# Optimization experiments

Measured on AMD Instinct MI355X. Metric: run time of the kernel, lower is better.

The kernel has to match this reference:

```python
import jax, jax.numpy as jnp
import numpy as np

B, S, D, H = 2, 2048, 1024, 16
HD = D // H  # head_dim = 64


def setup_inputs() -> dict:
    key = jax.random.key(0)
    ks = jax.random.split(key, 6)
    scale = D ** -0.5
    x = jax.random.normal(ks[0], (B, S, D), dtype=jnp.float32)
    wq = jax.random.normal(ks[1], (D, D), dtype=jnp.float32) * scale
    wk = jax.random.normal(ks[2], (D, D), dtype=jnp.float32) * scale
    wv = jax.random.normal(ks[3], (D, D), dtype=jnp.float32) * scale
    wo = jax.random.normal(ks[4], (D, D), dtype=jnp.float32) * scale
    # RoPE frequencies: theta_i = 10000^(-2i/HD), angles[t, i] = t * theta_i
    inv_freq = 1.0 / (10000.0 ** (np.arange(0, HD, 2, dtype=np.float32) / HD))
    t = np.arange(S, dtype=np.float32)
    angles = np.outer(t, inv_freq)  # [S, HD//2]
    freqs_cos = jnp.asarray(np.cos(angles), dtype=jnp.float32)
    freqs_sin = jnp.asarray(np.sin(angles), dtype=jnp.float32)
    # additive causal mask [1,1,S,S]
    neg = jnp.float32(-1e9)
    mask = jnp.triu(jnp.full((S, S), neg, dtype=jnp.float32), k=1)[None, None]
    return {"x": x, "wq": wq, "wk": wk, "wv": wv, "wo": wo,
            "freqs_cos": freqs_cos, "freqs_sin": freqs_sin,
            "mask": mask, "start_pos": 0}


def _apply_rope(q, freqs_cos, freqs_sin):
    # q: [B, S, H, HD] -> pairs (even, odd) rotated by angle per position
    b, s, h, hd = q.shape
    q2 = q.reshape(b, s, h, hd // 2, 2)
    qr, qi = q2[..., 0], q2[..., 1]
    c = freqs_cos[None, :, None, :]  # [1, S, 1, HD//2]
    sn = freqs_sin[None, :, None, :]
    out_r = qr * c - qi * sn
    out_i = qr * sn + qi * c
    return jnp.stack([out_r, out_i], axis=-1).reshape(b, s, h, hd)


def reference(x, wq, wk, wv, wo, freqs_cos, freqs_sin, mask, start_pos):
    b, s, _ = x.shape
    xq = (x @ wq).reshape(b, s, H, HD)
    xk = (x @ wk).reshape(b, s, H, HD)
    xv = (x @ wv).reshape(b, s, H, HD)
    xq = _apply_rope(xq, freqs_cos, freqs_sin)
    xk = _apply_rope(xk, freqs_cos, freqs_sin)
    # [B, H, S, HD]
    q = xq.transpose(0, 2, 1, 3)
    k = xk.transpose(0, 2, 1, 3)
    v = xv.transpose(0, 2, 1, 3)
    scores = jnp.einsum('bhqd,bhkd->bhqk', q, k) / jnp.sqrt(jnp.float32(HD))
    scores = scores + mask
    probs = jax.nn.softmax(scores.astype(jnp.float32), axis=-1).astype(q.dtype)
    out = jnp.einsum('bhqk,bhkd->bhqd', probs, v)
    out = out.transpose(0, 2, 1, 3).reshape(b, s, H * HD)
    return out @ wo
```

## Files before the change

### kernel.cpp

```cpp
#include <hip/hip_runtime.h>

typedef unsigned short u16;
typedef __bf16 bf16x8 __attribute__((ext_vector_type(8)));
typedef float f32x4 __attribute__((ext_vector_type(4)));

#define DD 1024
#define SS 2048
#define HH 16
#define HDIM 64

__device__ __forceinline__ u16 f2bf(float f) {
  union { float f; unsigned u; } x; x.f = f;
  unsigned r = x.u + 0x7FFFu + ((x.u >> 16) & 1u);
  return (u16)(r >> 16);
}

__device__ __forceinline__ u16 f2bf_s(float f) {
  unsigned r;
  asm("v_cvt_pk_bf16_f32 %0, %1, %2" : "=v"(r) : "v"(f), "v"(0.f));
  return (u16)r;
}

__device__ __forceinline__ void gload_lds16(const u16* g, u16* l) {
  __builtin_amdgcn_global_load_lds((const __attribute__((address_space(1))) void*)g,
                                   (__attribute__((address_space(3))) void*)l, 16, 0, 0);
}

__global__ __launch_bounds__(256) void cvt_x(const float* __restrict__ in, u16* __restrict__ out, int n) {
  int i = (blockIdx.x * 256 + threadIdx.x) * 4;
  if (i + 3 < n) {
    float4 v = *(const float4*)(in + i);
    out[i + 0] = f2bf(v.x);
    out[i + 1] = f2bf(v.y);
    out[i + 2] = f2bf(v.z);
    out[i + 3] = f2bf(v.w);
  }
}

__global__ __launch_bounds__(256) void transpose_w(const float* __restrict__ w0, const float* __restrict__ w1,
                                                   const float* __restrict__ w2, const float* __restrict__ w3,
                                                   u16* __restrict__ out) {
  __shared__ float t[32][33];
  const float* w = (blockIdx.z == 0) ? w0 : (blockIdx.z == 1) ? w1 : (blockIdx.z == 2) ? w2 : w3;
  u16* o = out + (size_t)blockIdx.z * DD * DD;
  int j0 = blockIdx.x * 32;
  int i0 = blockIdx.y * 32;
  int tx = threadIdx.x, ty = threadIdx.y;
#pragma unroll
  for (int r = ty; r < 32; r += 8)
    t[r][tx] = w[(size_t)(i0 + r) * DD + j0 + tx];
  __syncthreads();
#pragma unroll
  for (int r = ty; r < 32; r += 8)
    o[(size_t)(j0 + r) * DD + i0 + tx] = f2bf(t[tx][r]);
}

__global__ __launch_bounds__(512, 4) void gemm_qkv(const u16* __restrict__ xb, const u16* __restrict__ wT,
                                                   const float* __restrict__ fc, const float* __restrict__ fs,
                                                   u16* __restrict__ Qr, u16* __restrict__ Kr, u16* __restrict__ Vt) {
  __shared__ u16 As[2][128 * 64];
  __shared__ u16 Bs[2][192 * 64];
  const int tid = threadIdx.x;
  const int lane = tid & 63, wid = tid >> 6;
  const int wm = wid >> 2, wn = wid & 3;
  const int lr = lane & 15, lg = lane >> 4;
  const int m0 = blockIdx.x * 128, n0 = blockIdx.y * 192;

  f32x4 acc[4][3];
#pragma unroll
  for (int i = 0; i < 4; ++i)
#pragma unroll
    for (int j = 0; j < 3; ++j) acc[i][j] = (f32x4){0.f, 0.f, 0.f, 0.f};

  auto stage = [&](int buf, int k0) {
#pragma unroll
    for (int i = 0; i < 2; ++i) {
      int c = tid + i * 512;
      int row = c >> 3, j = (c & 7) ^ (row & 7);
      gload_lds16(xb + (size_t)(m0 + row) * DD + k0 + j * 8, &As[buf][c * 8]);
    }
#pragma unroll
    for (int i = 0; i < 3; ++i) {
      int c = tid + i * 512;
      int row = c >> 3, j = (c & 7) ^ (row & 7);
      gload_lds16(wT + (size_t)(n0 + row) * DD + k0 + j * 8, &Bs[buf][c * 8]);
    }
  };

  stage(0, 0);
  for (int kt = 0; kt < 16; ++kt) {
    const int cur = kt & 1;
    __syncthreads();
    if (kt < 15) stage(cur ^ 1, (kt + 1) * 64);
#pragma unroll
    for (int ks = 0; ks < 2; ++ks) {
      bf16x8 af[4], bfr[3];
#pragma unroll
      for (int mi = 0; mi < 4; ++mi) {
        int row = wm * 64 + mi * 16 + lr;
        int ch = (ks * 4 + lg) ^ (row & 7);
        af[mi] = *(const bf16x8*)(&As[cur][row * 64 + ch * 8]);
      }
#pragma unroll
      for (int ni = 0; ni < 3; ++ni) {
        int row = wn * 48 + ni * 16 + lr;
        int ch = (ks * 4 + lg) ^ (row & 7);
        bfr[ni] = *(const bf16x8*)(&Bs[cur][row * 64 + ch * 8]);
      }
      __builtin_amdgcn_s_setprio(1);
#pragma unroll
      for (int mi = 0; mi < 4; ++mi)
#pragma unroll
        for (int ni = 0; ni < 3; ++ni)
          acc[mi][ni] = __builtin_amdgcn_mfma_f32_16x16x32_bf16(af[mi], bfr[ni], acc[mi][ni], 0, 0, 0);
      __builtin_amdgcn_s_setprio(0);
    }
  }

#pragma unroll
  for (int mi = 0; mi < 4; ++mi)
#pragma unroll
    for (int ni = 0; ni < 3; ++ni) {
      const int nb = n0 + wn * 48 + ni * 16;
      const int z = nb >> 10;
      const int nn = (nb & 1023) + lr;
      const int h = nn >> 6, hd = nn & 63;
#pragma unroll
      for (int j = 0; j < 4; ++j) {
        int m = m0 + wm * 64 + mi * 16 + lg * 4 + j;
        float v = acc[mi][ni][j];
        int b = m >> 11, s = m & 2047;
        if (z == 2) {
          Vt[((size_t)(b * HH + h) * HDIM + hd) * SS + s] = f2bf(v);
        } else {
          float pv = __shfl_xor(v, 1);
          int fi = s * 32 + (hd >> 1);
          float c = fc[fi], sn = fs[fi];
          float o = ((hd & 1) == 0) ? (v * c - pv * sn) : (pv * sn + v * c);
          u16* dst = (z == 0) ? Qr : Kr;
          dst[((size_t)(b * HH + h) * SS + s) * HDIM + hd] = f2bf(o);
        }
      }
    }
}

__device__ __forceinline__ void stage_tile(const u16* __restrict__ Kh, const u16* __restrict__ Vh,
                                           int i2, u16* Kbuf, u16* Vbuf, int tid) {
#pragma unroll
  for (int k = 0; k < 2; ++k) {
    const int c = tid + k * 512;
    const int tt = c >> 9, cl = c & 511;
    const int row = cl >> 3, j = (cl & 7) ^ (row & 7);
    gload_lds16(Kh + (size_t)(i2 * 128 + tt * 64 + row) * HDIM + j * 8, Kbuf + c * 8);
    gload_lds16(Vh + (size_t)row * SS + i2 * 128 + tt * 64 + j * 8, Vbuf + c * 8);
  }
}

__device__ __forceinline__ void attn_pass(int qt, int bh, const u16* __restrict__ Qh,
                                          const u16* __restrict__ Kh, const u16* __restrict__ Vh,
                                          u16* __restrict__ Ob, u16* KbR, u16* VbR, u16* Pw,
                                          int gid, int wq) {
  const int tid = threadIdx.x;
  const int lane = tid & 63;
  const int lr = lane & 15, lg = lane >> 4;
  const int q0 = qt * 64 + wq * 16;

  bf16x8 aq[2];
#pragma unroll
  for (int ks = 0; ks < 2; ++ks)
    aq[ks] = *(const bf16x8*)(Qh + (q0 + lr) * HDIM + ks * 32 + lg * 8);

  bf16x8 ones;
  {
    union { u16 u[8]; bf16x8 v; } ou;
#pragma unroll
    for (int i = 0; i < 8; ++i) ou.u[i] = 0x3F80;
    ones = ou.v;
  }

  f32x4 o[4];
#pragma unroll
  for (int d = 0; d < 4; ++d) o[d] = (f32x4){0.f, 0.f, 0.f, 0.f};
  f32x4 ls = (f32x4){0.f, 0.f, 0.f, 0.f};

  const int n2 = (qt + 2) >> 1;

  __syncthreads();
  stage_tile(Kh, Vh, 0, KbR, VbR, tid);

  for (int i = 0; i < n2; ++i) {
    const int cur = i & 1;
    __syncthreads();
    if (i + 1 < n2) stage_tile(Kh, Vh, i + 1, KbR + (cur ^ 1) * 8192, VbR + (cur ^ 1) * 8192, tid);

    const int t = 2 * i + gid;
    const u16* Kt = KbR + cur * 8192 + gid * 4096;
    const u16* Vtl = VbR + cur * 8192 + gid * 4096;

    f32x4 sc[4];
#pragma unroll
    for (int kb = 0; kb < 4; ++kb) sc[kb] = (f32x4){0.f, 0.f, 0.f, 0.f};
    __builtin_amdgcn_s_setprio(1);
#pragma unroll
    for (int ks = 0; ks < 2; ++ks)
#pragma unroll
      for (int kb = 0; kb < 4; ++kb) {
        int row = kb * 16 + lr;
        int ch = (ks * 4 + lg) ^ (row & 7);
        bf16x8 bk = *(const bf16x8*)(Kt + row * 64 + ch * 8);
        sc[kb] = __builtin_amdgcn_mfma_f32_16x16x32_bf16(aq[ks], bk, sc[kb], 0, 0, 0);
      }
    __builtin_amdgcn_s_setprio(0);

    if (t >= qt) {
#pragma unroll
      for (int kb = 0; kb < 4; ++kb)
#pragma unroll
        for (int j = 0; j < 4; ++j) {
          int q = q0 + lg * 4 + j;
          int kk = t * 64 + kb * 16 + lr;
          float e = __expf(sc[kb][j] * 0.125f);
          sc[kb][j] = (kk > q) ? 0.f : e;
        }
    } else {
#pragma unroll
      for (int kb = 0; kb < 4; ++kb)
#pragma unroll
        for (int j = 0; j < 4; ++j)
          sc[kb][j] = __expf(sc[kb][j] * 0.125f);
    }

#pragma unroll
    for (int kb = 0; kb < 4; ++kb)
#pragma unroll
      for (int j = 0; j < 4; ++j) {
        int rr = lg * 4 + j;
        int ccol = kb * 16 + lr;
        int ch = (ccol >> 3) ^ (rr & 7);
        Pw[rr * 64 + ch * 8 + (ccol & 7)] = f2bf_s(sc[kb][j]);
      }
#pragma unroll
    for (int ks = 0; ks < 2; ++ks) {
      int chp = (ks * 4 + lg) ^ (lr & 7);
      bf16x8 ap = *(const bf16x8*)(Pw + lr * 64 + chp * 8);
      __builtin_amdgcn_s_setprio(1);
      ls = __builtin_amdgcn_mfma_f32_16x16x32_bf16(ap, ones, ls, 0, 0, 0);
#pragma unroll
      for (int d = 0; d < 4; ++d) {
        int row = d * 16 + lr;
        int ch = (ks * 4 + lg) ^ (row & 7);
        bf16x8 bv = *(const bf16x8*)(Vtl + row * 64 + ch * 8);
        o[d] = __builtin_amdgcn_mfma_f32_16x16x32_bf16(ap, bv, o[d], 0, 0, 0);
      }
      __builtin_amdgcn_s_setprio(0);
    }
  }

  __syncthreads();
  float* mo = (float*)KbR;
  float* ml = (float*)VbR;
  if (gid == 1) {
#pragma unroll
    for (int d = 0; d < 4; ++d)
#pragma unroll
      for (int j = 0; j < 4; ++j)
        mo[(wq * 16 + lg * 4 + j) * 64 + d * 16 + lr] = o[d][j];
    if (lr == 0) {
#pragma unroll
      for (int j = 0; j < 4; ++j) ml[wq * 16 + lg * 4 + j] = ls[j];
    }
  }
  __syncthreads();
  if (gid == 0) {
    const int b = bh >> 4, h = bh & 15;
#pragma unroll
    for (int j = 0; j < 4; ++j) ls[j] += ml[wq * 16 + lg * 4 + j];
#pragma unroll
    for (int d = 0; d < 4; ++d)
#pragma unroll
      for (int j = 0; j < 4; ++j) {
        float val = o[d][j] + mo[(wq * 16 + lg * 4 + j) * 64 + d * 16 + lr];
        int s = q0 + lg * 4 + j;
        int col = h * HDIM + d * 16 + lr;
        Ob[((size_t)b * SS + s) * DD + col] = f2bf(val / ls[j]);
      }
  }
}

__global__ __launch_bounds__(512, 4) void attn(const u16* __restrict__ Qr, const u16* __restrict__ Kr,
                                               const u16* __restrict__ Vt, u16* __restrict__ Ob) {
  __shared__ u16 Kb[2][2][64 * 64];
  __shared__ u16 Vb[2][2][64 * 64];
  __shared__ u16 Ps[8][16 * 64];
  const int id = blockIdx.x;
  const int xcd = id & 7;
  const int r = id >> 3;
  const int pair = r & 15;
  const int bh = xcd * 4 + (r >> 4);
  const u16* Qh = Qr + (size_t)bh * SS * HDIM;
  const u16* Kh = Kr + (size_t)bh * SS * HDIM;
  const u16* Vh = Vt + (size_t)bh * HDIM * SS;
  const int wid = threadIdx.x >> 6;
  const int gid = wid >> 2, wq = wid & 3;
  u16* Pw = &Ps[wid][0];
  attn_pass(pair, bh, Qh, Kh, Vh, Ob, &Kb[0][0][0], &Vb[0][0][0], Pw, gid, wq);
  attn_pass(31 - pair, bh, Qh, Kh, Vh, Ob, &Kb[0][0][0], &Vb[0][0][0], Pw, gid, wq);
}

__global__ __launch_bounds__(256, 2) void gemm_wo(const u16* __restrict__ Ab, const u16* __restrict__ woT,
                                                  float* __restrict__ out) {
  __shared__ u16 As[2][128 * 64];
  __shared__ u16 Bs[2][128 * 64];
  const int tid = threadIdx.x;
  const int lane = tid & 63, wid = tid >> 6;
  const int wm = wid >> 1, wn = wid & 1;
  const int lr = lane & 15, lg = lane >> 4;
  const int m0 = blockIdx.x * 128, n0 = blockIdx.y * 128;

  f32x4 acc[4][4];
#pragma unroll
  for (int i = 0; i < 4; ++i)
#pragma unroll
    for (int j = 0; j < 4; ++j) acc[i][j] = (f32x4){0.f, 0.f, 0.f, 0.f};

  auto stage = [&](int buf, int k0) {
#pragma unroll
    for (int i = 0; i < 4; ++i) {
      int c = i * 256 + tid;
      int row = c >> 3, j = (c & 7) ^ (row & 7);
      gload_lds16(Ab + (size_t)(m0 + row) * DD + k0 + j * 8, &As[buf][c * 8]);
      gload_lds16(woT + (size_t)(n0 + row) * DD + k0 + j * 8, &Bs[buf][c * 8]);
    }
  };

  stage(0, 0);
  for (int kt = 0; kt < 16; ++kt) {
    const int cur = kt & 1;
    __syncthreads();
    if (kt < 15) stage(cur ^ 1, (kt + 1) * 64);
#pragma unroll
    for (int ks = 0; ks < 2; ++ks) {
      bf16x8 af[4], bfr[4];
#pragma unroll
      for (int mi = 0; mi < 4; ++mi) {
        int row = wm * 64 + mi * 16 + lr;
        int ch = (ks * 4 + lg) ^ (row & 7);
        af[mi] = *(const bf16x8*)(&As[cur][row * 64 + ch * 8]);
      }
#pragma unroll
      for (int ni = 0; ni < 4; ++ni) {
        int row = wn * 64 + ni * 16 + lr;
        int ch = (ks * 4 + lg) ^ (row & 7);
        bfr[ni] = *(const bf16x8*)(&Bs[cur][row * 64 + ch * 8]);
      }
      __builtin_amdgcn_s_setprio(1);
#pragma unroll
      for (int mi = 0; mi < 4; ++mi)
#pragma unroll
        for (int ni = 0; ni < 4; ++ni)
          acc[mi][ni] = __builtin_amdgcn_mfma_f32_16x16x32_bf16(af[mi], bfr[ni], acc[mi][ni], 0, 0, 0);
      __builtin_amdgcn_s_setprio(0);
    }
  }

  const int lane2 = threadIdx.x & 63;
  (void)lane2;
#pragma unroll
  for (int mi = 0; mi < 4; ++mi)
#pragma unroll
    for (int ni = 0; ni < 4; ++ni)
#pragma unroll
      for (int j = 0; j < 4; ++j) {
        int m = m0 + wm * 64 + mi * 16 + lg * 4 + j;
        int n = n0 + wn * 64 + ni * 16 + lr;
        out[(size_t)m * DD + n] = acc[mi][ni][j];
      }
}

extern "C" void kernel_launch(void* const* d_in, const int* in_sizes, int n_in,
                              void* d_out, int out_size, void* d_ws, size_t ws_size,
                              hipStream_t stream) {
  const float* x  = (const float*)d_in[0];
  const float* wq = (const float*)d_in[1];
  const float* wk = (const float*)d_in[2];
  const float* wv = (const float*)d_in[3];
  const float* wo = (const float*)d_in[4];
  const float* fc = (const float*)d_in[5];
  const float* fs = (const float*)d_in[6];
  float* out = (float*)d_out;

  char* ws = (char*)d_ws;
  u16* xb = (u16*)(ws);
  u16* wT = (u16*)(ws + (8ull << 20));
  u16* Qr = (u16*)(ws + (16ull << 20));
  u16* Kr = (u16*)(ws + (24ull << 20));
  u16* Vt = (u16*)(ws + (32ull << 20));
  u16* Ob = (u16*)(ws + (40ull << 20));

  cvt_x<<<4096, 256, 0, stream>>>(x, xb, 4096 * 1024);
  transpose_w<<<dim3(32, 32, 4), dim3(32, 8), 0, stream>>>(wq, wk, wv, wo, wT);
  gemm_qkv<<<dim3(32, 16), 512, 0, stream>>>(xb, wT, fc, fs, Qr, Kr, Vt);
  attn<<<512, 512, 0, stream>>>(Qr, Kr, Vt, Ob);
  gemm_wo<<<dim3(32, 8), 256, 0, stream>>>(Ob, wT + 3ull * DD * DD, out);
}
```

Measured before the change: 118.6 us.

## Triple-buffer GEMM K-loops with vmcnt waits, fuse prep kernels, widen gemm_wo

Both GEMMs move from double to triple LDS buffering. Each iteration issues the next tile's global-to-LDS loads, waits only on the older tile with a partial s_waitcnt vmcnt, then does a single barrier, which removes one full sync and lets the load overlap the MFMA work. The x cast and weight-transpose kernels are merged into one launch to cut a kernel launch. gemm_wo goes from 256 to 512 threads with half the accumulators per wave. The trade-off is more LDS per block, which may lower occupancy (gemm_qkv's launch bound drops to 2 blocks per SM), and the hand-counted vmcnt values must match the number of loads issued.

```diff
diff --git a/kernel.cpp b/kernel.cpp
--- a/kernel.cpp
+++ b/kernel.cpp
@@ -26,26 +26,30 @@
                                    (__attribute__((address_space(3))) void*)l, 16, 0, 0);
 }
 
-__global__ __launch_bounds__(256) void cvt_x(const float* __restrict__ in, u16* __restrict__ out, int n) {
-  int i = (blockIdx.x * 256 + threadIdx.x) * 4;
-  if (i + 3 < n) {
-    float4 v = *(const float4*)(in + i);
-    out[i + 0] = f2bf(v.x);
-    out[i + 1] = f2bf(v.y);
-    out[i + 2] = f2bf(v.z);
-    out[i + 3] = f2bf(v.w);
-  }
-}
-
-__global__ __launch_bounds__(256) void transpose_w(const float* __restrict__ w0, const float* __restrict__ w1,
-                                                   const float* __restrict__ w2, const float* __restrict__ w3,
-                                                   u16* __restrict__ out) {
+__global__ __launch_bounds__(256) void prep(const float* __restrict__ x,
+                                            const float* __restrict__ w0, const float* __restrict__ w1,
+                                            const float* __restrict__ w2, const float* __restrict__ w3,
+                                            u16* __restrict__ xb, u16* __restrict__ wT) {
   __shared__ float t[32][33];
-  const float* w = (blockIdx.z == 0) ? w0 : (blockIdx.z == 1) ? w1 : (blockIdx.z == 2) ? w2 : w3;
-  u16* o = out + (size_t)blockIdx.z * DD * DD;
-  int j0 = blockIdx.x * 32;
-  int i0 = blockIdx.y * 32;
-  int tx = threadIdx.x, ty = threadIdx.y;
+  const int id = blockIdx.x;
+  const int tid = threadIdx.x;
+  if (id < 4096) {
+    int i = (id * 256 + tid) * 4;
+    float4 v = *(const float4*)(x + i);
+    xb[i + 0] = f2bf(v.x);
+    xb[i + 1] = f2bf(v.y);
+    xb[i + 2] = f2bf(v.z);
+    xb[i + 3] = f2bf(v.w);
+    return;
+  }
+  const int tt = id - 4096;
+  const int z = tt >> 10;
+  const int xy = tt & 1023;
+  const int j0 = (xy & 31) * 32;
+  const int i0 = (xy >> 5) * 32;
+  const float* w = (z == 0) ? w0 : (z == 1) ? w1 : (z == 2) ? w2 : w3;
+  u16* o = wT + (size_t)z * DD * DD;
+  const int tx = tid & 31, ty = tid >> 5;
 #pragma unroll
   for (int r = ty; r < 32; r += 8)
     t[r][tx] = w[(size_t)(i0 + r) * DD + j0 + tx];
@@ -55,11 +59,11 @@
     o[(size_t)(j0 + r) * DD + i0 + tx] = f2bf(t[tx][r]);
 }
 
-__global__ __launch_bounds__(512, 4) void gemm_qkv(const u16* __restrict__ xb, const u16* __restrict__ wT,
+__global__ __launch_bounds__(512, 2) void gemm_qkv(const u16* __restrict__ xb, const u16* __restrict__ wT,
                                                    const float* __restrict__ fc, const float* __restrict__ fs,
                                                    u16* __restrict__ Qr, u16* __restrict__ Kr, u16* __restrict__ Vt) {
-  __shared__ u16 As[2][128 * 64];
-  __shared__ u16 Bs[2][192 * 64];
+  __shared__ u16 As[3][128 * 64];
+  __shared__ u16 Bs[3][192 * 64];
   const int tid = threadIdx.x;
   const int lane = tid & 63, wid = tid >> 6;
   const int wm = wid >> 2, wn = wid & 3;
@@ -88,10 +92,17 @@
   };
 
   stage(0, 0);
+  int cur = 0;
   for (int kt = 0; kt < 16; ++kt) {
-    const int cur = kt & 1;
-    __syncthreads();
-    if (kt < 15) stage(cur ^ 1, (kt + 1) * 64);
+    if (kt < 15) {
+      int nxt = (cur == 2) ? 0 : cur + 1;
+      stage(nxt, (kt + 1) * 64);
+      asm volatile("s_waitcnt vmcnt(5)" ::: "memory");
+    } else {
+      asm volatile("s_waitcnt vmcnt(0)" ::: "memory");
+    }
+    __builtin_amdgcn_s_barrier();
+    __builtin_amdgcn_sched_barrier(0);
 #pragma unroll
     for (int ks = 0; ks < 2; ++ks) {
       bf16x8 af[4], bfr[3];
@@ -115,6 +126,7 @@
           acc[mi][ni] = __builtin_amdgcn_mfma_f32_16x16x32_bf16(af[mi], bfr[ni], acc[mi][ni], 0, 0, 0);
       __builtin_amdgcn_s_setprio(0);
     }
+    cur = (cur == 2) ? 0 : cur + 1;
   }
 
 #pragma unroll
@@ -307,26 +319,26 @@
   attn_pass(31 - pair, bh, Qh, Kh, Vh, Ob, &Kb[0][0][0], &Vb[0][0][0], Pw, gid, wq);
 }
 
-__global__ __launch_bounds__(256, 2) void gemm_wo(const u16* __restrict__ Ab, const u16* __restrict__ woT,
+__global__ __launch_bounds__(512, 2) void gemm_wo(const u16* __restrict__ Ab, const u16* __restrict__ woT,
                                                   float* __restrict__ out) {
-  __shared__ u16 As[2][128 * 64];
-  __shared__ u16 Bs[2][128 * 64];
+  __shared__ u16 As[3][128 * 64];
+  __shared__ u16 Bs[3][128 * 64];
   const int tid = threadIdx.x;
   const int lane = tid & 63, wid = tid >> 6;
   const int wm = wid >> 1, wn = wid & 1;
   const int lr = lane & 15, lg = lane >> 4;
   const int m0 = blockIdx.x * 128, n0 = blockIdx.y * 128;
 
-  f32x4 acc[4][4];
-#pragma unroll
-  for (int i = 0; i < 4; ++i)
+  f32x4 acc[2][4];
+#pragma unroll
+  for (int i = 0; i < 2; ++i)
 #pragma unroll
     for (int j = 0; j < 4; ++j) acc[i][j] = (f32x4){0.f, 0.f, 0.f, 0.f};
 
   auto stage = [&](int buf, int k0) {
 #pragma unroll
-    for (int i = 0; i < 4; ++i) {
-      int c = i * 256 + tid;
+    for (int i = 0; i < 2; ++i) {
+      int c = tid + i * 512;
       int row = c >> 3, j = (c & 7) ^ (row & 7);
       gload_lds16(Ab + (size_t)(m0 + row) * DD + k0 + j * 8, &As[buf][c * 8]);
       gload_lds16(woT + (size_t)(n0 + row) * DD + k0 + j * 8, &Bs[buf][c * 8]);
@@ -334,16 +346,23 @@
   };
 
   stage(0, 0);
+  int cur = 0;
   for (int kt = 0; kt < 16; ++kt) {
-    const int cur = kt & 1;
-    __syncthreads();
-    if (kt < 15) stage(cur ^ 1, (kt + 1) * 64);
+    if (kt < 15) {
+      int nxt = (cur == 2) ? 0 : cur + 1;
+      stage(nxt, (kt + 1) * 64);
+      asm volatile("s_waitcnt vmcnt(4)" ::: "memory");
+    } else {
+      asm volatile("s_waitcnt vmcnt(0)" ::: "memory");
+    }
+    __builtin_amdgcn_s_barrier();
+    __builtin_amdgcn_sched_barrier(0);
 #pragma unroll
     for (int ks = 0; ks < 2; ++ks) {
-      bf16x8 af[4], bfr[4];
-#pragma unroll
-      for (int mi = 0; mi < 4; ++mi) {
-        int row = wm * 64 + mi * 16 + lr;
+      bf16x8 af[2], bfr[4];
+#pragma unroll
+      for (int mi = 0; mi < 2; ++mi) {
+        int row = wm * 32 + mi * 16 + lr;
         int ch = (ks * 4 + lg) ^ (row & 7);
         af[mi] = *(const bf16x8*)(&As[cur][row * 64 + ch * 8]);
       }
@@ -355,23 +374,22 @@
       }
       __builtin_amdgcn_s_setprio(1);
 #pragma unroll
-      for (int mi = 0; mi < 4; ++mi)
+      for (int mi = 0; mi < 2; ++mi)
 #pragma unroll
         for (int ni = 0; ni < 4; ++ni)
           acc[mi][ni] = __builtin_amdgcn_mfma_f32_16x16x32_bf16(af[mi], bfr[ni], acc[mi][ni], 0, 0, 0);
       __builtin_amdgcn_s_setprio(0);
     }
-  }
-
-  const int lane2 = threadIdx.x & 63;
-  (void)lane2;
-#pragma unroll
-  for (int mi = 0; mi < 4; ++mi)
+    cur = (cur == 2) ? 0 : cur + 1;
+  }
+
+#pragma unroll
+  for (int mi = 0; mi < 2; ++mi)
 #pragma unroll
     for (int ni = 0; ni < 4; ++ni)
 #pragma unroll
       for (int j = 0; j < 4; ++j) {
-        int m = m0 + wm * 64 + mi * 16 + lg * 4 + j;
+        int m = m0 + wm * 32 + mi * 16 + lg * 4 + j;
         int n = n0 + wn * 64 + ni * 16 + lr;
         out[(size_t)m * DD + n] = acc[mi][ni][j];
       }
@@ -397,9 +415,8 @@
   u16* Vt = (u16*)(ws + (32ull << 20));
   u16* Ob = (u16*)(ws + (40ull << 20));
 
-  cvt_x<<<4096, 256, 0, stream>>>(x, xb, 4096 * 1024);
-  transpose_w<<<dim3(32, 32, 4), dim3(32, 8), 0, stream>>>(wq, wk, wv, wo, wT);
+  prep<<<8192, 256, 0, stream>>>(x, wq, wk, wv, wo, xb, wT);
   gemm_qkv<<<dim3(32, 16), 512, 0, stream>>>(xb, wT, fc, fs, Qr, Kr, Vt);
   attn<<<512, 512, 0, stream>>>(Qr, Kr, Vt, Ob);
-  gemm_wo<<<dim3(32, 8), 256, 0, stream>>>(Ob, wT + 3ull * DD * DD, out);
-}
+  gemm_wo<<<dim3(32, 8), 512, 0, stream>>>(Ob, wT + 3ull * DD * DD, out);
+}
```

New measurement: 115.9 us. -2.3%, faster.
